# Kernel optimization log

Measured on AMD Instinct MI355X. Metric: run time of the kernel, lower is better.

The kernel has to match this reference:

```python
import jax, jax.numpy as jnp
import numpy as np

B = 65536

def setup_inputs() -> dict:
    key = jax.random.key(0)
    ks = jax.random.split(key, 6)
    x = jax.random.normal(ks[0], (B, 784), dtype=jnp.float32)
    w_conv = jnp.ones((3, 3), dtype=jnp.float32)  # Parameter(ones((3,3)))
    w1 = jax.random.normal(ks[1], (676, 256), dtype=jnp.float32) * 0.04
    b1 = jax.random.normal(ks[2], (256,), dtype=jnp.float32) * 0.01
    w2 = jax.random.normal(ks[3], (256, 10), dtype=jnp.float32) * 0.06
    b2 = jax.random.normal(ks[4], (10,), dtype=jnp.float32) * 0.01
    return {"x": x, "w_conv": w_conv, "w1": w1, "b1": b1, "w2": w2, "b2": b2}

def reference(x, w_conv, w1, b1, w2, b2):
    b = x.shape[0]
    img = x.reshape(b, 1, 28, 28)
    # Convolve() is cross-correlation (no kernel flip), 'VALID': 28->26
    kern = w_conv.reshape(1, 1, 3, 3)
    conv = jax.lax.conv_general_dilated(
        img, kern, window_strides=(1, 1), padding='VALID',
        dimension_numbers=('NCHW', 'OIHW', 'NCHW'))  # (B,1,26,26)
    feat = conv.reshape(b, 676)
    h = jax.nn.relu(feat @ w1 + b1)  # (B,256)
    return h @ w2 + b2               # (B,10)
```

## Files before the change

kernel.cpp:

```cpp
#include <hip/hip_runtime.h>
#include <hip/hip_bf16.h>
#include <stdint.h>

typedef __bf16 bf16;
typedef __attribute__((ext_vector_type(8))) __bf16 bf16x8;
typedef __attribute__((ext_vector_type(4))) float f32x4;

#define KREAL 784
#define KPAD  800

#define GLOBAL_AS __attribute__((address_space(1)))
#define LDS_AS    __attribute__((address_space(3)))

__global__ __launch_bounds__(256) void prep_w1t(const float* __restrict__ w_conv,
                                                const float* __restrict__ w1,
                                                bf16* __restrict__ W1t) {
    const int k = blockIdx.x;
    const int n = threadIdx.x;
    float s = 0.0f;
    if (k < KREAL) {
        const int r = k / 28, c = k % 28;
        #pragma unroll
        for (int di = 0; di < 3; ++di) {
            const int i = r - di;
            if (i < 0 || i >= 26) continue;
            #pragma unroll
            for (int dj = 0; dj < 3; ++dj) {
                const int j = c - dj;
                if (j < 0 || j >= 26) continue;
                s += w_conv[di * 3 + dj] * w1[(i * 26 + j) * 256 + n];
            }
        }
    }
    W1t[n * KPAD + k] = (bf16)s;
}

__global__ __launch_bounds__(256, 2) void fused_mlp(
    const float* __restrict__ x,
    const bf16*  __restrict__ W1t,
    const float* __restrict__ b1,
    const float* __restrict__ w2,
    const float* __restrict__ b2,
    float* __restrict__ out)
{
    __shared__ bf16  Bs[256][32];
    __shared__ float w2s[256][10];
    __shared__ float b1s[256];
    __shared__ float b2s[10];

    const int t    = threadIdx.x;
    const int wave = t >> 6;
    const int lane = t & 63;
    const int c    = lane & 15;
    const int q    = lane >> 4;

    const int row0 = blockIdx.x * 128;

    for (int i = t; i < 2560; i += 256) ((float*)w2s)[i] = w2[i];
    b1s[t] = b1[t];
    if (t < 10) b2s[t] = b2[t];

    const float* arow0 = x + (size_t)(row0 + wave * 32 + c) * KREAL + q * 8;
    const float* arow1 = arow0 + (size_t)16 * KREAL;

    const bf16* bsrc0 = W1t + (size_t)(wave * 64 + (lane >> 2)) * KPAD + (lane & 3) * 8;
    char* bdst0 = (char*)(&Bs[0][0]) + wave * 4096;

    f32x4 acc[2][16];
    #pragma unroll
    for (int mt = 0; mt < 2; ++mt)
        #pragma unroll
        for (int nt = 0; nt < 16; ++nt)
            acc[mt][nt] = (f32x4){0.f, 0.f, 0.f, 0.f};

    #pragma unroll 1
    for (int k0 = 0; k0 < KPAD; k0 += 32) {
        __syncthreads();

        #pragma unroll
        for (int j = 0; j < 4; ++j) {
            __builtin_amdgcn_global_load_lds(
                (const GLOBAL_AS void*)(bsrc0 + k0 + j * 16 * KPAD),
                (LDS_AS void*)(bdst0 + j * 1024), 16, 0, 0);
        }

        float4 f0a, f0b, f1a, f1b;
        if (k0 + q * 8 < KREAL) {
            const float* p0 = arow0 + k0;
            const float* p1 = arow1 + k0;
            f0a = *(const float4*)p0; f0b = *(const float4*)(p0 + 4);
            f1a = *(const float4*)p1; f1b = *(const float4*)(p1 + 4);
        } else {
            f0a = f0b = f1a = f1b = (float4){0.f, 0.f, 0.f, 0.f};
        }
        bf16x8 a0, a1;
        a0[0] = (bf16)f0a.x; a0[1] = (bf16)f0a.y; a0[2] = (bf16)f0a.z; a0[3] = (bf16)f0a.w;
        a0[4] = (bf16)f0b.x; a0[5] = (bf16)f0b.y; a0[6] = (bf16)f0b.z; a0[7] = (bf16)f0b.w;
        a1[0] = (bf16)f1a.x; a1[1] = (bf16)f1a.y; a1[2] = (bf16)f1a.z; a1[3] = (bf16)f1a.w;
        a1[4] = (bf16)f1b.x; a1[5] = (bf16)f1b.y; a1[6] = (bf16)f1b.z; a1[7] = (bf16)f1b.w;

        __syncthreads();

        #pragma unroll
        for (int nt = 0; nt < 16; ++nt) {
            bf16x8 b = *(const bf16x8*)&Bs[nt * 16 + c][q * 8];
            acc[0][nt] = __builtin_amdgcn_mfma_f32_16x16x32_bf16(a0, b, acc[0][nt], 0, 0, 0);
            acc[1][nt] = __builtin_amdgcn_mfma_f32_16x16x32_bf16(a1, b, acc[1][nt], 0, 0, 0);
        }
    }

    float bl[16];
    #pragma unroll
    for (int nt = 0; nt < 16; ++nt) bl[nt] = b1s[nt * 16 + c];

    #pragma unroll
    for (int mt = 0; mt < 2; ++mt)
        #pragma unroll
        for (int nt = 0; nt < 16; ++nt)
            #pragma unroll
            for (int r = 0; r < 4; ++r) {
                float v = acc[mt][nt][r] + bl[nt];
                acc[mt][nt][r] = v > 0.f ? v : 0.f;
            }

    #pragma unroll 1
    for (int j = 0; j < 10; ++j) {
        float wj[16];
        #pragma unroll
        for (int nt = 0; nt < 16; ++nt) wj[nt] = w2s[nt * 16 + c][j];
        const float b2j = b2s[j];
        #pragma unroll
        for (int mt = 0; mt < 2; ++mt)
            #pragma unroll
            for (int r = 0; r < 4; ++r) {
                float s = 0.f;
                #pragma unroll
                for (int nt = 0; nt < 16; ++nt) s += acc[mt][nt][r] * wj[nt];
                s += __shfl_xor(s, 1, 64);
                s += __shfl_xor(s, 2, 64);
                s += __shfl_xor(s, 4, 64);
                s += __shfl_xor(s, 8, 64);
                if (c == j) {
                    const int row = row0 + wave * 32 + mt * 16 + q * 4 + r;
                    out[(size_t)row * 10 + j] = s + b2j;
                }
            }
    }
}

extern "C" void kernel_launch(void* const* d_in, const int* in_sizes, int n_in,
                              void* d_out, int out_size, void* d_ws, size_t ws_size,
                              hipStream_t stream) {
    const float* x  = (const float*)d_in[0];
    const float* wc = (const float*)d_in[1];
    const float* w1 = (const float*)d_in[2];
    const float* b1 = (const float*)d_in[3];
    const float* w2 = (const float*)d_in[4];
    const float* b2 = (const float*)d_in[5];
    float* out = (float*)d_out;
    bf16* W1t = (bf16*)d_ws;

    prep_w1t<<<dim3(KPAD), dim3(256), 0, stream>>>(wc, w1, W1t);
    fused_mlp<<<dim3(65536 / 128), dim3(256), 0, stream>>>(x, W1t, b1, w2, b2, out);
}
```

Measured before the change: 317.9 us.

## Double-buffer W1 tiles in LDS with padded tile-contiguous layout and prefetch

The prep kernel now stores the folded conv+W1 weights as 25 contiguous tiles of 256x40 bf16, padded from a row stride of 32 to 40 to cut LDS bank conflicts. The main loop double-buffers these tiles in LDS and prefetches the next tile and the next x fragment while the MFMAs run on the current one, so there is one barrier per iteration instead of two. LDS use per block grows from one 16 KB tile to two 20 KB tiles, and more registers stay live for the prefetched x values, which may reduce occupancy.

```diff
diff --git a/kernel.cpp b/kernel.cpp
--- a/kernel.cpp
+++ b/kernel.cpp
@@ -7,18 +7,22 @@
 typedef __attribute__((ext_vector_type(4))) float f32x4;
 
 #define KREAL 784
-#define KPAD  800
+#define NTILES 25
+#define TROW   40
+#define TILE_ELEMS (256 * TROW)
 
 #define GLOBAL_AS __attribute__((address_space(1)))
 #define LDS_AS    __attribute__((address_space(3)))
 
-__global__ __launch_bounds__(256) void prep_w1t(const float* __restrict__ w_conv,
-                                                const float* __restrict__ w1,
-                                                bf16* __restrict__ W1t) {
-    const int k = blockIdx.x;
-    const int n = threadIdx.x;
+__global__ __launch_bounds__(256) void prep_w1tt(const float* __restrict__ w_conv,
+                                                 const float* __restrict__ w1,
+                                                 bf16* __restrict__ W) {
+    const int tile = blockIdx.x / TROW;
+    const int kk   = blockIdx.x % TROW;
+    const int n    = threadIdx.x;
+    const int k    = tile * 32 + kk;
     float s = 0.0f;
-    if (k < KREAL) {
+    if (kk < 32 && k < KREAL) {
         const int r = k / 28, c = k % 28;
         #pragma unroll
         for (int di = 0; di < 3; ++di) {
@@ -32,18 +36,18 @@
             }
         }
     }
-    W1t[n * KPAD + k] = (bf16)s;
+    W[(size_t)tile * TILE_ELEMS + n * TROW + kk] = (bf16)s;
 }
 
 __global__ __launch_bounds__(256, 2) void fused_mlp(
     const float* __restrict__ x,
-    const bf16*  __restrict__ W1t,
+    const bf16*  __restrict__ W,
     const float* __restrict__ b1,
     const float* __restrict__ w2,
     const float* __restrict__ b2,
     float* __restrict__ out)
 {
-    __shared__ bf16  Bs[256][32];
+    __shared__ bf16  Bs[2][TILE_ELEMS];
     __shared__ float w2s[256][10];
     __shared__ float b1s[256];
     __shared__ float b2s[10];
@@ -62,9 +66,7 @@
 
     const float* arow0 = x + (size_t)(row0 + wave * 32 + c) * KREAL + q * 8;
     const float* arow1 = arow0 + (size_t)16 * KREAL;
-
-    const bf16* bsrc0 = W1t + (size_t)(wave * 64 + (lane >> 2)) * KPAD + (lane & 3) * 8;
-    char* bdst0 = (char*)(&Bs[0][0]) + wave * 4096;
+    const bf16* bsrc = W + (size_t)(wave * 5) * 512 + lane * 8;
 
     f32x4 acc[2][16];
     #pragma unroll
@@ -73,40 +75,61 @@
         for (int nt = 0; nt < 16; ++nt)
             acc[mt][nt] = (f32x4){0.f, 0.f, 0.f, 0.f};
 
+    #pragma unroll
+    for (int j = 0; j < 5; ++j) {
+        __builtin_amdgcn_global_load_lds(
+            (const GLOBAL_AS void*)(bsrc + j * 512),
+            (LDS_AS void*)((char*)&Bs[0][0] + (wave * 5 + j) * 1024), 16, 0, 0);
+    }
+    float4 f0a = *(const float4*)arow0, f0b = *(const float4*)(arow0 + 4);
+    float4 f1a = *(const float4*)arow1, f1b = *(const float4*)(arow1 + 4);
+    bf16x8 a0, a1;
+    a0[0] = (bf16)f0a.x; a0[1] = (bf16)f0a.y; a0[2] = (bf16)f0a.z; a0[3] = (bf16)f0a.w;
+    a0[4] = (bf16)f0b.x; a0[5] = (bf16)f0b.y; a0[6] = (bf16)f0b.z; a0[7] = (bf16)f0b.w;
+    a1[0] = (bf16)f1a.x; a1[1] = (bf16)f1a.y; a1[2] = (bf16)f1a.z; a1[3] = (bf16)f1a.w;
+    a1[4] = (bf16)f1b.x; a1[5] = (bf16)f1b.y; a1[6] = (bf16)f1b.z; a1[7] = (bf16)f1b.w;
+    __syncthreads();
+
     #pragma unroll 1
-    for (int k0 = 0; k0 < KPAD; k0 += 32) {
-        __syncthreads();
+    for (int it = 0; it < NTILES; ++it) {
+        const int cur = it & 1;
+        const bool more = (it + 1) < NTILES;
 
-        #pragma unroll
-        for (int j = 0; j < 4; ++j) {
-            __builtin_amdgcn_global_load_lds(
-                (const GLOBAL_AS void*)(bsrc0 + k0 + j * 16 * KPAD),
-                (LDS_AS void*)(bdst0 + j * 1024), 16, 0, 0);
+        if (more) {
+            const bf16* bs = bsrc + (size_t)(it + 1) * TILE_ELEMS;
+            char* bd = (char*)&Bs[cur ^ 1][0] + wave * 5 * 1024;
+            #pragma unroll
+            for (int j = 0; j < 5; ++j) {
+                __builtin_amdgcn_global_load_lds(
+                    (const GLOBAL_AS void*)(bs + j * 512),
+                    (LDS_AS void*)(bd + j * 1024), 16, 0, 0);
+            }
+            const int kn = (it + 1) * 32;
+            if (kn + q * 8 < KREAL) {
+                const float* p0 = arow0 + kn;
+                const float* p1 = arow1 + kn;
+                f0a = *(const float4*)p0; f0b = *(const float4*)(p0 + 4);
+                f1a = *(const float4*)p1; f1b = *(const float4*)(p1 + 4);
+            } else {
+                f0a = f0b = f1a = f1b = (float4){0.f, 0.f, 0.f, 0.f};
+            }
         }
-
-        float4 f0a, f0b, f1a, f1b;
-        if (k0 + q * 8 < KREAL) {
-            const float* p0 = arow0 + k0;
-            const float* p1 = arow1 + k0;
-            f0a = *(const float4*)p0; f0b = *(const float4*)(p0 + 4);
-            f1a = *(const float4*)p1; f1b = *(const float4*)(p1 + 4);
-        } else {
-            f0a = f0b = f1a = f1b = (float4){0.f, 0.f, 0.f, 0.f};
-        }
-        bf16x8 a0, a1;
-        a0[0] = (bf16)f0a.x; a0[1] = (bf16)f0a.y; a0[2] = (bf16)f0a.z; a0[3] = (bf16)f0a.w;
-        a0[4] = (bf16)f0b.x; a0[5] = (bf16)f0b.y; a0[6] = (bf16)f0b.z; a0[7] = (bf16)f0b.w;
-        a1[0] = (bf16)f1a.x; a1[1] = (bf16)f1a.y; a1[2] = (bf16)f1a.z; a1[3] = (bf16)f1a.w;
-        a1[4] = (bf16)f1b.x; a1[5] = (bf16)f1b.y; a1[6] = (bf16)f1b.z; a1[7] = (bf16)f1b.w;
-
-        __syncthreads();
 
         #pragma unroll
         for (int nt = 0; nt < 16; ++nt) {
-            bf16x8 b = *(const bf16x8*)&Bs[nt * 16 + c][q * 8];
+            bf16x8 b = *(const bf16x8*)&Bs[cur][(nt * 16 + c) * TROW + q * 8];
             acc[0][nt] = __builtin_amdgcn_mfma_f32_16x16x32_bf16(a0, b, acc[0][nt], 0, 0, 0);
             acc[1][nt] = __builtin_amdgcn_mfma_f32_16x16x32_bf16(a1, b, acc[1][nt], 0, 0, 0);
         }
+
+        if (more) {
+            a0[0] = (bf16)f0a.x; a0[1] = (bf16)f0a.y; a0[2] = (bf16)f0a.z; a0[3] = (bf16)f0a.w;
+            a0[4] = (bf16)f0b.x; a0[5] = (bf16)f0b.y; a0[6] = (bf16)f0b.z; a0[7] = (bf16)f0b.w;
+            a1[0] = (bf16)f1a.x; a1[1] = (bf16)f1a.y; a1[2] = (bf16)f1a.z; a1[3] = (bf16)f1a.w;
+            a1[4] = (bf16)f1b.x; a1[5] = (bf16)f1b.y; a1[6] = (bf16)f1b.z; a1[7] = (bf16)f1b.w;
+        }
+
+        __syncthreads();
     }
 
     float bl[16];
@@ -158,8 +181,8 @@
     const float* w2 = (const float*)d_in[4];
     const float* b2 = (const float*)d_in[5];
     float* out = (float*)d_out;
-    bf16* W1t = (bf16*)d_ws;
+    bf16* W = (bf16*)d_ws;
 
-    prep_w1t<<<dim3(KPAD), dim3(256), 0, stream>>>(wc, w1, W1t);
-    fused_mlp<<<dim3(65536 / 128), dim3(256), 0, stream>>>(x, W1t, b1, w2, b2, out);
+    prep_w1tt<<<dim3(NTILES * TROW), dim3(256), 0, stream>>>(wc, w1, W);
+    fused_mlp<<<dim3(65536 / 128), dim3(256), 0, stream>>>(x, W, b1, w2, b2, out);
 }
```

Result: no change. 317.0 us (-0.3%).
